# Performance work log

Measured on AMD Instinct MI355X. Metric: run time of the kernel, lower is better.

The kernel has to match this reference:

```python
import jax, jax.numpy as jnp
import numpy as np

N_EMBD = 1024
N_HEAD = 16
HEAD_SIZE = 64


def setup_inputs() -> dict:
    key = jax.random.key(0)
    ks = jax.random.split(key, 6)
    B, T, C, H, D = 2, 2048, N_EMBD, N_HEAD, HEAD_SIZE
    s = 1.0 / np.sqrt(C)
    x = jax.random.normal(ks[0], (B, T, C), dtype=jnp.float32)
    Wq = jax.random.normal(ks[1], (H, C, D), dtype=jnp.float32) * s
    Wk = jax.random.normal(ks[2], (H, C, D), dtype=jnp.float32) * s
    Wv = jax.random.normal(ks[3], (H, C, D), dtype=jnp.float32) * s
    Wo = jax.random.normal(ks[4], (H * D, C), dtype=jnp.float32) * (1.0 / np.sqrt(H * D))
    bo = jax.random.normal(ks[5], (C,), dtype=jnp.float32) * 0.01
    return {"x": x, "Wq": Wq, "Wk": Wk, "Wv": Wv, "Wo": Wo, "bo": bo}


def reference(x, Wq, Wk, Wv, Wo, bo):
    B, T, C = x.shape
    H, _, D = Wq.shape
    # Per-head projections, batched across heads: [B,H,T,D]
    q = jnp.einsum('btc,hcd->bhtd', x, Wq)
    k = jnp.einsum('btc,hcd->bhtd', x, Wk)
    v = jnp.einsum('btc,hcd->bhtd', x, Wv)
    # NOTE: original scales by sqrt(C) = sqrt(n_embd), not sqrt(head_size)
    scale = 1.0 / jnp.sqrt(jnp.float32(C))
    att = jnp.einsum('bhtd,bhsd->bhts', q, k) * scale  # [B,H,T,T]
    causal = jnp.tril(jnp.ones((T, T), dtype=bool))
    att = jnp.where(causal, att, -jnp.inf)
    att = jax.nn.softmax(att, axis=-1)
    # dropout omitted (eval mode / deterministic reference)
    out = jnp.einsum('bhts,bhsd->bhtd', att, v)  # [B,H,T,D]
    out = out.transpose(0, 2, 1, 3).reshape(B, T, H * D)
    return out @ Wo + bo
```

## Files before the change

kernel.cpp:

```cpp
#include <hip/hip_runtime.h>
#include <hip/hip_bf16.h>


typedef __hip_bfloat16 bf16;
typedef __bf16 v8bf __attribute__((ext_vector_type(8)));
typedef float  v4f  __attribute__((ext_vector_type(4)));
typedef unsigned long long u64;
typedef unsigned int u32;

#define MFMA16(a, b, c) __builtin_amdgcn_mfma_f32_16x16x32_bf16((a), (b), (c), 0, 0, 0)

__device__ __forceinline__ bf16 f2b(float x) { return __float2bfloat16(x); }
__device__ __forceinline__ __bf16 f2braw(float x) {
  bf16 t = __float2bfloat16(x);
  return *reinterpret_cast<__bf16*>(&t);
}
__device__ __forceinline__ unsigned short f2bu(float x) {
  bf16 t = __float2bfloat16(x);
  return *reinterpret_cast<unsigned short*>(&t);
}

__device__ __forceinline__ void load16_lds(const bf16* gptr, const bf16* lptr) {
  __builtin_amdgcn_global_load_lds(
      (const __attribute__((address_space(1))) u32*)gptr,
      (__attribute__((address_space(3))) u32*)lptr, 16, 0, 0);
}

__global__ __launch_bounds__(256) void prep_kernel(
    const float* __restrict__ x,
    const float* __restrict__ Wq, const float* __restrict__ Wk,
    const float* __restrict__ Wv, const float* __restrict__ Wo,
    bf16* __restrict__ xb, bf16* __restrict__ wt, bf16* __restrict__ wot)
{
  __shared__ float Lt[32][33];
  const int bid = blockIdx.x, tid = threadIdx.x;

  if (bid < 2048) {
    size_t i = ((size_t)bid * 256 + tid) * 8;
    float4 f0 = *(const float4*)(x + i);
    float4 f1 = *(const float4*)(x + i + 4);
    v8bf v;
    v[0] = f2braw(f0.x); v[1] = f2braw(f0.y); v[2] = f2braw(f0.z); v[3] = f2braw(f0.w);
    v[4] = f2braw(f1.x); v[5] = f2braw(f1.y); v[6] = f2braw(f1.z); v[7] = f2braw(f1.w);
    *(v8bf*)(xb + i) = v;
    return;
  }
  const int tx = tid & 31, ty = tid >> 5;
  if (bid < 5120) {
    const int idx = bid - 2048;
    const int z = idx >> 6, rem = idx & 63;
    const int p = z >> 4, h = z & 15;
    const float* ib = ((p == 0) ? Wq : (p == 1) ? Wk : Wv) + (size_t)h * 65536;
    bf16* ob = wt + (size_t)z * 65536;
    const int j0 = (rem & 1) * 32, i0 = (rem >> 1) * 32;
    #pragma unroll
    for (int r = 0; r < 4; ++r)
      Lt[ty + 8 * r][tx] = ib[(size_t)(i0 + ty + 8 * r) * 64 + j0 + tx];
    __syncthreads();
    #pragma unroll
    for (int r = 0; r < 4; ++r)
      ob[(size_t)(j0 + ty + 8 * r) * 1024 + i0 + tx] = f2b(Lt[tx][ty + 8 * r]);
  } else {
    const int idx = bid - 5120;
    const int j0 = (idx & 31) * 32, i0 = (idx >> 5) * 32;
    #pragma unroll
    for (int r = 0; r < 4; ++r)
      Lt[ty + 8 * r][tx] = Wo[(size_t)(i0 + ty + 8 * r) * 1024 + j0 + tx];
    __syncthreads();
    #pragma unroll
    for (int r = 0; r < 4; ++r)
      wot[(size_t)(j0 + ty + 8 * r) * 1024 + i0 + tx] = f2b(Lt[tx][ty + 8 * r]);
  }
}

__global__ __launch_bounds__(512, 2) void qkv_gemm_kernel(
    const bf16* __restrict__ xb, const bf16* __restrict__ wt,
    bf16* __restrict__ qkv)
{
  __shared__ __align__(16) bf16 Ash[3][256][32];
  __shared__ __align__(16) bf16 Bsh[3][256][32];

  const int mt = blockIdx.x, nt = blockIdx.y;
  const int tid = threadIdx.x, wid = tid >> 6, lane = tid & 63;
  const int ln = lane & 15, quad = lane >> 4;
  const int wm = wid >> 1, wn = wid & 1;
  const int m0 = mt * 256, n0 = nt * 192;

  const v4f vzero = {0.f, 0.f, 0.f, 0.f};
  v4f acc[4][6];
  #pragma unroll
  for (int mf = 0; mf < 4; ++mf)
    #pragma unroll
    for (int nf = 0; nf < 6; ++nf) acc[mf][nf] = vzero;

  const int srow = lane >> 2;
  const int sseg = ((lane & 3) ^ ((lane >> 3) & 3)) * 8;
  const int arow = wid * 32 + srow;
  const int br0 = wid * 32 + srow,  brow0 = (br0 < 192) ? br0 : 191;
  const int br1 = wid * 32 + 16 + srow, brow1 = (br1 < 192) ? br1 : 191;
  const bf16* ga  = xb + (size_t)(m0 + arow) * 1024 + sseg;
  const bf16* gb0 = wt + (size_t)(n0 + brow0) * 1024 + sseg;
  const bf16* gb1 = wt + (size_t)(n0 + brow1) * 1024 + sseg;

  const int fseg = (quad ^ ((ln >> 1) & 3)) * 8;

  #define QSTAGE(BUF) {                                          \
    load16_lds(ga,              &Ash[BUF][wid * 32][0]);         \
    load16_lds(ga + 16 * 1024,  &Ash[BUF][wid * 32 + 16][0]);    \
    load16_lds(gb0,             &Bsh[BUF][wid * 32][0]);         \
    load16_lds(gb1,             &Bsh[BUF][wid * 32 + 16][0]);    \
    ga += 32; gb0 += 32; gb1 += 32; }

  QSTAGE(0)
  QSTAGE(1)

  #define QSTEP(BUF, VM, DOSTAGE)                                          \
  {                                                                        \
    asm volatile("s_waitcnt vmcnt(" #VM ") lgkmcnt(0)" ::: "memory");      \
    __builtin_amdgcn_s_barrier();                                          \
    __builtin_amdgcn_sched_barrier(0);                                     \
    v8bf af[4], bfv[6];                                                    \
    _Pragma("unroll")                                                      \
    for (int mf = 0; mf < 4; ++mf)                                         \
      af[mf] = *(const v8bf*)&Ash[BUF][wm * 64 + mf * 16 + ln][fseg];      \
    _Pragma("unroll")                                                      \
    for (int nf = 0; nf < 6; ++nf)                                         \
      bfv[nf] = *(const v8bf*)&Bsh[BUF][wn * 96 + nf * 16 + ln][fseg];     \
    if (DOSTAGE) QSTAGE((BUF + 2) % 3)                                     \
    __builtin_amdgcn_s_setprio(1);                                         \
    _Pragma("unroll")                                                      \
    for (int mf = 0; mf < 4; ++mf)                                         \
      _Pragma("unroll")                                                    \
      for (int nf = 0; nf < 6; ++nf)                                       \
        acc[mf][nf] = MFMA16(af[mf], bfv[nf], acc[mf][nf]);                \
    __builtin_amdgcn_s_setprio(0);                                         \
  }

  #pragma unroll 1
  for (int it = 0; it < 10; ++it) {
    QSTEP(0, 4, 1)
    QSTEP(1, 4, 1)
    QSTEP(2, 4, 1)
  }
  QSTEP(0, 4, 0)
  QSTEP(1, 0, 0)
  #undef QSTEP
  #undef QSTAGE

  #pragma unroll
  for (int nf = 0; nf < 6; ++nf) {
    const int j = n0 + wn * 96 + nf * 16 + ln;
    const int p = j >> 10;
    const int h = (j >> 6) & 15;
    const int d = j & 63;
    if (p < 2) {
      const float scale = (p == 0) ? 0.0450841149f : 1.0f;
      bf16* base = qkv + (size_t)p * 4194304 + (size_t)h * 262144;
      #pragma unroll
      for (int mf = 0; mf < 4; ++mf)
        #pragma unroll
        for (int r = 0; r < 4; ++r) {
          int m = m0 + wm * 64 + mf * 16 + quad * 4 + r;
          base[(size_t)m * 64 + d] = f2b(acc[mf][nf][r] * scale);
        }
    } else {
      bf16* vb = qkv + (size_t)2 * 4194304 + (size_t)h * 262144;
      #pragma unroll
      for (int mf = 0; mf < 4; ++mf) {
        int mrow = m0 + wm * 64 + mf * 16 + quad * 4;
        int bi = mrow >> 11, t0 = mrow & 2047;
        u64 pk = (u64)f2bu(acc[mf][nf][0]) |
                 ((u64)f2bu(acc[mf][nf][1]) << 16) |
                 ((u64)f2bu(acc[mf][nf][2]) << 32) |
                 ((u64)f2bu(acc[mf][nf][3]) << 48);
        *(u64*)(vb + (size_t)bi * 131072 + (size_t)d * 2048 + t0) = pk;
      }
    }
  }
}

__global__ __launch_bounds__(256, 4) void attn_kernel(
    const bf16* __restrict__ qkv, bf16* __restrict__ att)
{
  union ShU {
    struct { bf16 K[2][64][64]; bf16 V[2][64][64]; } t;
    struct { float O[2][64][36]; float L[2][36]; } c;
  };
  __shared__ __align__(16) ShU sh;

  const int fid = blockIdx.x;
  const int j = fid >> 5;
  const int jr = j & 7, jq = j >> 3;
  const int mt = (jq == 0) ? (31 - jr) : (jq == 1) ? (8 + jr)
               : (jq == 2) ? (23 - jr) : jr;
  const int grp = fid & 31;
  const int b = grp >> 4, h = grp & 15;

  const int tid = threadIdx.x, w = tid >> 6, lane = tid & 63;
  const int ln = lane & 15, quad = lane >> 4;
  const int qh = w & 1, kh = w >> 1;

  const bf16* qbase  = qkv + (size_t)h * 262144 + (size_t)b * 131072;
  const bf16* kbase  = qbase + 4194304;
  const bf16* vtbase = qbase + 8388608;

  const int l8 = lane & 7, r8 = lane >> 3;
  const int slot = l8 ^ r8;
  const int p0 = w * 16 + r8, p1 = p0 + 8;
  const int kp0 = (p0 & 32) | ((p0 & 12) << 1) | ((p0 & 16) >> 2) | (p0 & 3);
  const int kp1 = (p1 & 32) | ((p1 & 12) << 1) | ((p1 & 16) >> 2) | (p1 & 3);
  const bf16* gkp0 = kbase + kp0 * 64 + slot * 8;
  const bf16* gkp1 = kbase + kp1 * 64 + slot * 8;
  const bf16* gvp0 = vtbase + p0 * 2048 + slot * 8;
  const bf16* gvp1 = gvp0 + 8 * 2048;

  const int sw = ln & 7;
  const int cc0 = ((quad    ) ^ sw) * 8;
  const int cc1 = ((quad + 4) ^ sw) * 8;
  const int cck = kh ? cc1 : cc0;
  const int krow0 = (kh * 32 + ln) * 64;
  const int ka0 = krow0 + cc0, ka1 = krow0 + cc1;
  const int voff = ln * 64 + cck;

  v8bf vone;
  {
    unsigned short u = 0x3F80;
    __bf16 e = *reinterpret_cast<__bf16*>(&u);
    #pragma unroll
    for (int jj = 0; jj < 8; ++jj) vone[jj] = e;
  }
  const v4f vzero = {0.f, 0.f, 0.f, 0.f};
  const float NEG = -30000.0f;

  #define STAGE2(BUF) {                                          \
    load16_lds(gkp0, &sh.t.K[BUF][w * 16][0]);                   \
    load16_lds(gkp1, &sh.t.K[BUF][w * 16 + 8][0]);               \
    load16_lds(gvp0, &sh.t.V[BUF][w * 16][0]);                   \
    load16_lds(gvp1, &sh.t.V[BUF][w * 16 + 8][0]);               \
    gkp0 += 4096; gkp1 += 4096; gvp0 += 64; gvp1 += 64; }

  const int row0 = mt * 64;
  const int qrow = row0 + qh * 32;

  v8bf aq[2][2];
  #pragma unroll
  for (int mc = 0; mc < 2; ++mc)
    #pragma unroll
    for (int ks = 0; ks < 2; ++ks)
      aq[mc][ks] = *(const v8bf*)(qbase +
          (size_t)(qrow + mc * 16 + ln) * 64 + ks * 32 + quad * 8);

  v4f o[2][4], lacc[2];
  #pragma unroll
  for (int mc = 0; mc < 2; ++mc) {
    lacc[mc] = vzero;
    #pragma unroll
    for (int dt = 0; dt < 4; ++dt) o[mc][dt] = vzero;
  }

  const int kb_end = mt;
  int kb = 0;
  STAGE2(0)

  #define TILE(BUF)                                                        \
  {                                                                        \
    __syncthreads();                                    \
    const bf16* krB = &sh.t.K[BUF][0][0];                                  \
    const bf16* vrB = &sh.t.V[BUF][0][0];                                  \
    v8bf kf[2][2], vf[4];                                                  \
    kf[0][0] = *(const v8bf*)(krB + ka0);                                  \
    kf[1][0] = *(const v8bf*)(krB + ka1);                                  \
    kf[0][1] = *(const v8bf*)(krB + ka0 + 1024);                           \
    kf[1][1] = *(const v8bf*)(krB + ka1 + 1024);                           \
    vf[0] = *(const v8bf*)(vrB + voff);                                    \
    vf[1] = *(const v8bf*)(vrB + voff + 1024);                             \
    vf[2] = *(const v8bf*)(vrB + voff + 2048);                             \
    vf[3] = *(const v8bf*)(vrB + voff + 3072);                             \
    if (kb < kb_end) STAGE2(BUF ^ 1)                                       \
    _Pragma("unroll")                                                      \
    for (int mc = 0; mc < 2; ++mc) {                                       \
      __builtin_amdgcn_s_setprio(1);                                       \
      v4f s[2];                                                            \
      s[0] = vzero; s[1] = vzero;                                          \
      _Pragma("unroll")                                                    \
      for (int ks = 0; ks < 2; ++ks) {                                     \
        s[0] = MFMA16(kf[ks][0], aq[mc][ks], s[0]);                        \
        s[1] = MFMA16(kf[ks][1], aq[mc][ks], s[1]);                        \
      }                                                                    \
      __builtin_amdgcn_s_setprio(0);                                       \
      const int qg = qrow + mc * 16 + ln;                                  \
      if (kb == kb_end) {                      \
        _Pragma("unroll")                                                  \
        for (int nfl = 0; nfl < 2; ++nfl) {                                \
          const int kc = kb * 64 + kh * 32 + quad * 8 + nfl * 4;           \
          _Pragma("unroll")                                                \
          for (int r = 0; r < 4; ++r)                                      \
            if (kc + r > qg) s[nfl][r] = NEG;                              \
        }                                                                  \
      }                                                                    \
      float ex[2][4];                                                      \
      _Pragma("unroll")                                                    \
      for (int nfl = 0; nfl < 2; ++nfl)                                    \
        _Pragma("unroll")                                                  \
        for (int r = 0; r < 4; ++r)                                        \
          ex[nfl][r] = exp2f(s[nfl][r]);                                   \
      union { u32 uw[4]; v8bf v; } pu;                                     \
      _Pragma("unroll")                                                    \
      for (int nfl = 0; nfl < 2; ++nfl)                                    \
        _Pragma("unroll")                                                  \
        for (int wi = 0; wi < 2; ++wi)                                     \
          asm("v_cvt_pk_bf16_f32 %0, %1, %2"                               \
              : "=v"(pu.uw[nfl * 2 + wi])                                  \
              : "v"(ex[nfl][2 * wi]), "v"(ex[nfl][2 * wi + 1]));           \
      __builtin_amdgcn_s_setprio(1);                                       \
      lacc[mc] = MFMA16(pu.v, vone, lacc[mc]);                             \
      _Pragma("unroll")                                                    \
      for (int dt = 0; dt < 4; ++dt)                                       \
        o[mc][dt] = MFMA16(pu.v, vf[dt], o[mc][dt]);                       \
      __builtin_amdgcn_s_setprio(0);                                       \
    }                                                                      \
  }

  while (true) {
    TILE(0)
    if (kb >= kb_end) break;
    ++kb;
    TILE(1)
    if (kb >= kb_end) break;
    ++kb;
  }
  #undef TILE
  #undef STAGE2

  __syncthreads();
  if (kh == 1) {
    #pragma unroll
    for (int mc = 0; mc < 2; ++mc) {
      #pragma unroll
      for (int dt = 0; dt < 4; ++dt)
        *(v4f*)&sh.c.O[qh][dt * 16 + ln][mc * 16 + quad * 4] = o[mc][dt];
      if (ln == 0)
        *(v4f*)&sh.c.L[qh][mc * 16 + quad * 4] = lacc[mc];
    }
  }
  __syncthreads();
  if (kh == 0) {
    #pragma unroll
    for (int mc = 0; mc < 2; ++mc) {
      v4f pl = *(const v4f*)&sh.c.L[qh][mc * 16 + quad * 4];
      v4f inv;
      #pragma unroll
      for (int r = 0; r < 4; ++r) inv[r] = 1.0f / (lacc[mc][r] + pl[r]);
      #pragma unroll
      for (int dt = 0; dt < 4; ++dt) {
        v4f po = *(const v4f*)&sh.c.O[qh][dt * 16 + ln][mc * 16 + quad * 4];
        #pragma unroll
        for (int r = 0; r < 4; ++r) {
          int m = b * 2048 + qrow + mc * 16 + quad * 4 + r;
          att[(size_t)m * 1024 + h * 64 + dt * 16 + ln] =
              f2b((o[mc][dt][r] + po[r]) * inv[r]);
        }
      }
    }
  }
}

__global__ __launch_bounds__(256) void out_gemm_kernel(
    const bf16* __restrict__ att, const bf16* __restrict__ wot,
    const float* __restrict__ bo, float* __restrict__ out)
{
  __shared__ __align__(16) bf16 Ash[3][128][32];
  __shared__ __align__(16) bf16 Bsh[3][64][32];

  const int mt = blockIdx.x, nt = blockIdx.y;
  const int tid = threadIdx.x, w = tid >> 6, lane = tid & 63;
  const int ln = lane & 15, quad = lane >> 4;
  const int wm = w >> 1, wn = w & 1;
  const int m0 = mt * 128, n0 = nt * 64;

  const v4f vzero = {0.f, 0.f, 0.f, 0.f};
  v4f acc[4][2];
  #pragma unroll
  for (int mf = 0; mf < 4; ++mf)
    #pragma unroll
    for (int nf = 0; nf < 2; ++nf) acc[mf][nf] = vzero;

  const int srow = lane >> 2;
  const int sseg = ((lane & 3) ^ ((lane >> 3) & 3)) * 8;
  const bf16* ga = att + (size_t)(m0 + 32 * w + srow) * 1024 + sseg;
  const bf16* gb = wot + (size_t)(n0 + 16 * w + srow) * 1024 + sseg;

  const int fseg = (quad ^ ((ln >> 1) & 3)) * 8;

  #define OSTAGE(BUF) {                                          \
    load16_lds(ga,             &Ash[BUF][32 * w][0]);            \
    load16_lds(ga + 16 * 1024, &Ash[BUF][32 * w + 16][0]);       \
    load16_lds(gb,             &Bsh[BUF][16 * w][0]);            \
    ga += 32; gb += 32; }

  OSTAGE(0)
  OSTAGE(1)

  #define OSTEP(BUF, VM, DOSTAGE)                                          \
  {                                                                        \
    asm volatile("s_waitcnt vmcnt(" #VM ") lgkmcnt(0)" ::: "memory");      \
    __builtin_amdgcn_s_barrier();                                          \
    __builtin_amdgcn_sched_barrier(0);                                     \
    v8bf af[4], bfv[2];                                                    \
    _Pragma("unroll")                                                      \
    for (int mf = 0; mf < 4; ++mf)                                         \
      af[mf] = *(const v8bf*)&Ash[BUF][wm * 64 + mf * 16 + ln][fseg];      \
    _Pragma("unroll")                                                      \
    for (int nf = 0; nf < 2; ++nf)                                         \
      bfv[nf] = *(const v8bf*)&Bsh[BUF][wn * 32 + nf * 16 + ln][fseg];     \
    if (DOSTAGE) OSTAGE((BUF + 2) % 3)                                     \
    __builtin_amdgcn_s_setprio(1);                                         \
    _Pragma("unroll")                                                      \
    for (int mf = 0; mf < 4; ++mf)                                         \
      _Pragma("unroll")                                                    \
      for (int nf = 0; nf < 2; ++nf)                                       \
        acc[mf][nf] = MFMA16(af[mf], bfv[nf], acc[mf][nf]);                \
    __builtin_amdgcn_s_setprio(0);                                         \
  }

  #pragma unroll 1
  for (int it = 0; it < 10; ++it) {
    OSTEP(0, 3, 1)
    OSTEP(1, 3, 1)
    OSTEP(2, 3, 1)
  }
  OSTEP(0, 3, 0)
  OSTEP(1, 0, 0)
  #undef OSTEP
  #undef OSTAGE

  #pragma unroll
  for (int nf = 0; nf < 2; ++nf) {
    int j = n0 + wn * 32 + nf * 16 + ln;
    float bias = bo[j];
    #pragma unroll
    for (int mf = 0; mf < 4; ++mf)
      #pragma unroll
      for (int r = 0; r < 4; ++r) {
        int m = m0 + wm * 64 + mf * 16 + quad * 4 + r;
        out[(size_t)m * 1024 + j] = acc[mf][nf][r] + bias;
      }
  }
}

extern "C" void kernel_launch(void* const* d_in, const int* in_sizes, int n_in,
                              void* d_out, int out_size, void* d_ws, size_t ws_size,
                              hipStream_t stream) {
  const float* x  = (const float*)d_in[0];
  const float* Wq = (const float*)d_in[1];
  const float* Wk = (const float*)d_in[2];
  const float* Wv = (const float*)d_in[3];
  const float* Wo = (const float*)d_in[4];
  const float* bo = (const float*)d_in[5];
  float* out = (float*)d_out;

  bf16* xb  = (bf16*)d_ws;
  bf16* wt  = xb + 4194304;
  bf16* wot = xb + 7340032;
  bf16* qkv = xb + 8388608;
  bf16* att = xb + 20971520;

  prep_kernel<<<6144, 256, 0, stream>>>(x, Wq, Wk, Wv, Wo, xb, wt, wot);
  qkv_gemm_kernel<<<dim3(16, 16), 512, 0, stream>>>(xb, wt, qkv);
  attn_kernel<<<1024, 256, 0, stream>>>(qkv, att);
  out_gemm_kernel<<<dim3(32, 16), 256, 0, stream>>>(att, wot, bo, out);
}
```

Before: 163.2 us.

## Restructure QKV GEMM to double-buffered K=64 tiles with four-phase MFMA interleave

Changes the QKV projection GEMM from a triple-buffered K=32 pipeline to a double-buffered K=64 pipeline. Each tile is split into four compute phases, and the A and B stage loads are issued in the first two phases so they overlap with MFMA work. The LDS layout moves to 64-wide rows with an 8-way XOR swizzle. This halves the number of outer barriers per K step but adds intra-tile barriers and a full vmcnt(0) wait at each tile boundary, which may reduce overlap compared with the three-stage prefetch.

```diff
diff --git a/kernel.cpp b/kernel.cpp
--- a/kernel.cpp
+++ b/kernel.cpp
@@ -77,8 +77,8 @@
     const bf16* __restrict__ xb, const bf16* __restrict__ wt,
     bf16* __restrict__ qkv)
 {
-  __shared__ __align__(16) bf16 Ash[3][256][32];
-  __shared__ __align__(16) bf16 Bsh[3][256][32];
+  __shared__ __align__(16) bf16 Ash[2][256][64];
+  __shared__ __align__(16) bf16 Bsh[2][192][64];
 
   const int mt = blockIdx.x, nt = blockIdx.y;
   const int tid = threadIdx.x, wid = tid >> 6, lane = tid & 63;
@@ -93,59 +93,124 @@
     #pragma unroll
     for (int nf = 0; nf < 6; ++nf) acc[mf][nf] = vzero;
 
-  const int srow = lane >> 2;
-  const int sseg = ((lane & 3) ^ ((lane >> 3) & 3)) * 8;
-  const int arow = wid * 32 + srow;
-  const int br0 = wid * 32 + srow,  brow0 = (br0 < 192) ? br0 : 191;
-  const int br1 = wid * 32 + 16 + srow, brow1 = (br1 < 192) ? br1 : 191;
-  const bf16* ga  = xb + (size_t)(m0 + arow) * 1024 + sseg;
-  const bf16* gb0 = wt + (size_t)(n0 + brow0) * 1024 + sseg;
-  const bf16* gb1 = wt + (size_t)(n0 + brow1) * 1024 + sseg;
-
-  const int fseg = (quad ^ ((ln >> 1) & 3)) * 8;
-
-  #define QSTAGE(BUF) {                                          \
-    load16_lds(ga,              &Ash[BUF][wid * 32][0]);         \
-    load16_lds(ga + 16 * 1024,  &Ash[BUF][wid * 32 + 16][0]);    \
-    load16_lds(gb0,             &Bsh[BUF][wid * 32][0]);         \
-    load16_lds(gb1,             &Bsh[BUF][wid * 32 + 16][0]);    \
-    ga += 32; gb0 += 32; gb1 += 32; }
-
-  QSTAGE(0)
-  QSTAGE(1)
-
-  #define QSTEP(BUF, VM, DOSTAGE)                                          \
+  const int r8 = lane >> 3, slot = (lane & 7) ^ r8;
+  const bf16* gA0 = xb + (size_t)(m0 + (wid * 4 + 0) * 8 + r8) * 1024 + slot * 8;
+  const bf16* gA1 = xb + (size_t)(m0 + (wid * 4 + 1) * 8 + r8) * 1024 + slot * 8;
+  const bf16* gA2 = xb + (size_t)(m0 + (wid * 4 + 2) * 8 + r8) * 1024 + slot * 8;
+  const bf16* gA3 = xb + (size_t)(m0 + (wid * 4 + 3) * 8 + r8) * 1024 + slot * 8;
+  const bf16* gB0 = wt + (size_t)(n0 + (wid * 3 + 0) * 8 + r8) * 1024 + slot * 8;
+  const bf16* gB1 = wt + (size_t)(n0 + (wid * 3 + 1) * 8 + r8) * 1024 + slot * 8;
+  const bf16* gB2 = wt + (size_t)(n0 + (wid * 3 + 2) * 8 + r8) * 1024 + slot * 8;
+
+  const int sw = ln & 7;
+  const int fs0 = ((quad    ) ^ sw) * 8;
+  const int fs1 = ((quad + 4) ^ sw) * 8;
+  const int arow = (wm * 64 + ln) * 64;
+  const int brow = (wn * 96 + ln) * 64;
+
+  #define STAGE_A(BUF) {                                         \
+    load16_lds(gA0, &Ash[BUF][(wid * 4 + 0) * 8][0]);            \
+    load16_lds(gA1, &Ash[BUF][(wid * 4 + 1) * 8][0]);            \
+    load16_lds(gA2, &Ash[BUF][(wid * 4 + 2) * 8][0]);            \
+    load16_lds(gA3, &Ash[BUF][(wid * 4 + 3) * 8][0]);            \
+    gA0 += 64; gA1 += 64; gA2 += 64; gA3 += 64; }
+  #define STAGE_B(BUF) {                                         \
+    load16_lds(gB0, &Bsh[BUF][(wid * 3 + 0) * 8][0]);            \
+    load16_lds(gB1, &Bsh[BUF][(wid * 3 + 1) * 8][0]);            \
+    load16_lds(gB2, &Bsh[BUF][(wid * 3 + 2) * 8][0]);            \
+    gB0 += 64; gB1 += 64; gB2 += 64; }
+
+  #define PHASE_SYNC() {                                         \
+    __builtin_amdgcn_s_barrier();                                \
+    asm volatile("s_waitcnt lgkmcnt(0)" ::: "memory");           \
+    __builtin_amdgcn_sched_barrier(0); }
+
+  #define QTILE(BUF, DOSTAGE, DOBOUND)                                     \
   {                                                                        \
-    asm volatile("s_waitcnt vmcnt(" #VM ") lgkmcnt(0)" ::: "memory");      \
-    __builtin_amdgcn_s_barrier();                                          \
-    __builtin_amdgcn_sched_barrier(0);                                     \
-    v8bf af[4], bfv[6];                                                    \
-    _Pragma("unroll")                                                      \
-    for (int mf = 0; mf < 4; ++mf)                                         \
-      af[mf] = *(const v8bf*)&Ash[BUF][wm * 64 + mf * 16 + ln][fseg];      \
-    _Pragma("unroll")                                                      \
-    for (int nf = 0; nf < 6; ++nf)                                         \
-      bfv[nf] = *(const v8bf*)&Bsh[BUF][wn * 96 + nf * 16 + ln][fseg];     \
-    if (DOSTAGE) QSTAGE((BUF + 2) % 3)                                     \
+    const bf16* aB = &Ash[BUF][0][0];                                      \
+    const bf16* bB = &Bsh[BUF][0][0];                                      \
+    v8bf af[4], bv[3];                                                     \
+                              \
+    _Pragma("unroll")                                                      \
+    for (int mf = 0; mf < 4; ++mf)                                         \
+      af[mf] = *(const v8bf*)(aB + arow + mf * 1024 + fs0);                \
+    _Pragma("unroll")                                                      \
+    for (int nf = 0; nf < 3; ++nf)                                         \
+      bv[nf] = *(const v8bf*)(bB + brow + nf * 1024 + fs0);                \
+    if (DOSTAGE) STAGE_A(BUF ^ 1)                                          \
+    PHASE_SYNC()                                                           \
     __builtin_amdgcn_s_setprio(1);                                         \
     _Pragma("unroll")                                                      \
     for (int mf = 0; mf < 4; ++mf)                                         \
       _Pragma("unroll")                                                    \
-      for (int nf = 0; nf < 6; ++nf)                                       \
-        acc[mf][nf] = MFMA16(af[mf], bfv[nf], acc[mf][nf]);                \
+      for (int nf = 0; nf < 3; ++nf)                                       \
+        acc[mf][nf] = MFMA16(af[mf], bv[nf], acc[mf][nf]);                 \
     __builtin_amdgcn_s_setprio(0);                                         \
-  }
+                                        \
+    _Pragma("unroll")                                                      \
+    for (int nf = 0; nf < 3; ++nf)                                         \
+      bv[nf] = *(const v8bf*)(bB + brow + (nf + 3) * 1024 + fs0);          \
+    if (DOSTAGE) STAGE_B(BUF ^ 1)                                          \
+    PHASE_SYNC()                                                           \
+    __builtin_amdgcn_s_setprio(1);                                         \
+    _Pragma("unroll")                                                      \
+    for (int mf = 0; mf < 4; ++mf)                                         \
+      _Pragma("unroll")                                                    \
+      for (int nf = 0; nf < 3; ++nf)                                       \
+        acc[mf][nf + 3] = MFMA16(af[mf], bv[nf], acc[mf][nf + 3]);         \
+    __builtin_amdgcn_s_setprio(0);                                         \
+                                            \
+    _Pragma("unroll")                                                      \
+    for (int mf = 0; mf < 4; ++mf)                                         \
+      af[mf] = *(const v8bf*)(aB + arow + mf * 1024 + fs1);                \
+    _Pragma("unroll")                                                      \
+    for (int nf = 0; nf < 3; ++nf)                                         \
+      bv[nf] = *(const v8bf*)(bB + brow + nf * 1024 + fs1);                \
+    PHASE_SYNC()                                                           \
+    __builtin_amdgcn_s_setprio(1);                                         \
+    _Pragma("unroll")                                                      \
+    for (int mf = 0; mf < 4; ++mf)                                         \
+      _Pragma("unroll")                                                    \
+      for (int nf = 0; nf < 3; ++nf)                                       \
+        acc[mf][nf] = MFMA16(af[mf], bv[nf], acc[mf][nf]);                 \
+    __builtin_amdgcn_s_setprio(0);                                         \
+                                                      \
+    _Pragma("unroll")                                                      \
+    for (int nf = 0; nf < 3; ++nf)                                         \
+      bv[nf] = *(const v8bf*)(bB + brow + (nf + 3) * 1024 + fs1);          \
+    PHASE_SYNC()                                                           \
+    __builtin_amdgcn_s_setprio(1);                                         \
+    _Pragma("unroll")                                                      \
+    for (int mf = 0; mf < 4; ++mf)                                         \
+      _Pragma("unroll")                                                    \
+      for (int nf = 0; nf < 3; ++nf)                                       \
+        acc[mf][nf + 3] = MFMA16(af[mf], bv[nf], acc[mf][nf + 3]);         \
+    __builtin_amdgcn_s_setprio(0);                                         \
+        \
+    if (DOBOUND) {                                                         \
+      asm volatile("s_waitcnt vmcnt(0) lgkmcnt(0)" ::: "memory");          \
+      __builtin_amdgcn_s_barrier();                                        \
+      __builtin_amdgcn_sched_barrier(0);                                   \
+    }                                                                      \
+  }
+
+  STAGE_A(0)
+  STAGE_B(0)
+  asm volatile("s_waitcnt vmcnt(0)" ::: "memory");
+  __builtin_amdgcn_s_barrier();
+  __builtin_amdgcn_sched_barrier(0);
 
   #pragma unroll 1
-  for (int it = 0; it < 10; ++it) {
-    QSTEP(0, 4, 1)
-    QSTEP(1, 4, 1)
-    QSTEP(2, 4, 1)
-  }
-  QSTEP(0, 4, 0)
-  QSTEP(1, 0, 0)
-  #undef QSTEP
-  #undef QSTAGE
+  for (int it = 0; it < 7; ++it) {
+    QTILE(0, 1, 1)
+    QTILE(1, 1, 1)
+  }
+  QTILE(0, 1, 1)
+  QTILE(1, 0, 0)
+  #undef QTILE
+  #undef PHASE_SYNC
+  #undef STAGE_A
+  #undef STAGE_B
 
   #pragma unroll
   for (int nf = 0; nf < 6; ++nf) {
```

Result: no change. 163.3 us (+0.1%).
